# Optimization experiments

Hardware: AMD Instinct MI355X
Metric: run time of the kernel (lower is better)

Reference implementation:

```python
import jax, jax.numpy as jnp
import numpy as np

H = 64
VOCAB = 64
READ_FREQ = 16


def setup_inputs() -> dict:
    key = jax.random.key(0)
    ks = jax.random.split(key, 16)
    B, L, M = 512, 2048, 256
    seq = jax.random.randint(ks[0], (B, L), 0, VOCAB)
    memory = jax.random.normal(ks[1], (B, M, H), dtype=jnp.float32)
    s = 0.1
    return {
        "seq": seq,
        "memory": memory,
        "embed_w": jax.random.normal(ks[2], (VOCAB, H), jnp.float32) * s,
        "gru_w_ih": jax.random.normal(ks[3], (3 * H, 2 * H), jnp.float32) * s,
        "gru_w_hh": jax.random.normal(ks[4], (3 * H, H), jnp.float32) * s,
        "gru_b_ih": jax.random.normal(ks[5], (3 * H,), jnp.float32) * s,
        "gru_b_hh": jax.random.normal(ks[6], (3 * H,), jnp.float32) * s,
        "key_w": jax.random.normal(ks[7], (H, H), jnp.float32) * s,
        "key_b": jax.random.normal(ks[8], (H,), jnp.float32) * s,
        "val_w": jax.random.normal(ks[9], (H, H), jnp.float32) * s,
        "val_b": jax.random.normal(ks[10], (H,), jnp.float32) * s,
        "query_w": jax.random.normal(ks[11], (H, H), jnp.float32) * s,
        "query_b": jax.random.normal(ks[12], (H,), jnp.float32) * s,
        "head_w": jax.random.normal(ks[13], (VOCAB, H), jnp.float32) * s,
        "head_b": jax.random.normal(ks[14], (VOCAB,), jnp.float32) * s,
    }


def _forward(seq, memory, embed_w, gru_w_ih, gru_w_hh, gru_b_ih, gru_b_hh,
             key_w, key_b, val_w, val_b, query_w, query_b, head_w, head_b):
    B, L = seq.shape
    scale = 1.0 / (H ** 0.5)
    # memory is fixed: precompute keys/values once (B, M, H)
    k = jnp.einsum("bmh,kh->bmk", memory, key_w) + key_b
    v = jnp.einsum("bmh,kh->bmk", memory, val_w) + val_b
    # embed all tokens up front: (B, L, H) -> chunks (C, F, B, H)
    emb = embed_w[seq]
    C = L // READ_FREQ
    emb_chunks = emb.reshape(B, C, READ_FREQ, H).transpose(1, 2, 0, 3)

    def gru_step(carry, x_t):
        h, retrieved = carry
        inp = jnp.concatenate([x_t, retrieved], axis=-1)  # (B, 2H)
        gi = inp @ gru_w_ih.T + gru_b_ih                   # (B, 3H)
        gh = h @ gru_w_hh.T + gru_b_hh                     # (B, 3H)
        i_r, i_z, i_n = jnp.split(gi, 3, axis=-1)
        h_r, h_z, h_n = jnp.split(gh, 3, axis=-1)
        r = jax.nn.sigmoid(i_r + h_r)
        z = jax.nn.sigmoid(i_z + h_z)
        n = jnp.tanh(i_n + r * h_n)
        h_new = (1.0 - z) * n + z * h
        return (h_new, retrieved), None

    def chunk_step(h, chunk_emb):  # chunk_emb: (READ_FREQ, B, H)
        q = h @ query_w.T + query_b                        # (B, H)
        scores = jnp.einsum("bh,bmh->bm", q, k) * scale
        w = jax.nn.softmax(scores, axis=-1)
        retrieved = jnp.einsum("bm,bmh->bh", w, v)
        (h, _), _ = jax.lax.scan(gru_step, (h, retrieved), chunk_emb)
        return h, None

    h0 = jnp.zeros((B, H), dtype=memory.dtype)
    h, _ = jax.lax.scan(chunk_step, h0, emb_chunks)
    return h @ head_w.T + head_b                            # (B, VOCAB)


def reference(seq, memory, embed_w, gru_w_ih, gru_w_hh, gru_b_ih, gru_b_hh,
              key_w, key_b, val_w, val_b, query_w, query_b, head_w, head_b):
    return _forward(seq, memory, embed_w, gru_w_ih, gru_w_hh, gru_b_ih, gru_b_hh,
                    key_w, key_b, val_w, val_b, query_w, query_b, head_w, head_b)
```

## Files before the change

kernel.cpp:

```cpp
#include <hip/hip_runtime.h>
#include <hip/hip_fp16.h>


#define B_ 512
#define L_ 2048
#define M_ 256
#define H_ 64
#define C_ 128
#define F_ 16

typedef float v2f __attribute__((ext_vector_type(2)));
typedef _Float16 h2v __attribute__((ext_vector_type(2)));

#if __has_builtin(__builtin_amdgcn_fdot2)
__device__ __forceinline__ float FDOT2(h2v a, h2v b, float c) {
    return __builtin_amdgcn_fdot2(a, b, c, false);
}
#else
__device__ __forceinline__ float FDOT2(h2v a, h2v b, float c) {
    return c + (float)a[0]*(float)b[0] + (float)a[1]*(float)b[1];
}
#endif

__device__ __forceinline__ h2v bch(unsigned u) { return __builtin_bit_cast(h2v, u); }
__device__ __forceinline__ unsigned rl_u(unsigned v, int lane) {
    return (unsigned)__builtin_amdgcn_readlane((int)v, lane);
}
__device__ __forceinline__ float rl(float v, int lane) {
    return __int_as_float(__builtin_amdgcn_readlane(__float_as_int(v), lane));
}
__device__ __forceinline__ unsigned pkrtz(float a, float b) {
    auto r = __builtin_amdgcn_cvt_pkrtz(a, b);
    return __builtin_bit_cast(unsigned, r);
}
__device__ __forceinline__ float dot4(float4 a, float4 b) {
    return a.x*b.x + a.y*b.y + a.z*b.z + a.w*b.w;
}
__device__ __forceinline__ float fast_rcp(float x) { return __builtin_amdgcn_rcpf(x); }
__device__ __forceinline__ float sigm(float x) { return fast_rcp(1.f + __expf(-x)); }
__device__ __forceinline__ float tanh_f(float x) {
    float e2 = __expf(-2.f * fabsf(x));
    return copysignf((1.f - e2) * fast_rcp(1.f + e2), x);
}
__device__ __forceinline__ unsigned h2rn(float a, float b) {
    __half2 h = __floats2half2_rn(a, b);
    return __builtin_bit_cast(unsigned, h);
}

#define WS_KT    0u
#define WS_V     16777216u
#define WS_G     33554432u
#define WS_WPHH  33603584u
#define WS_WR    33628160u
#define WS_QP    33652736u
#define WS_KWP   33660928u
#define WS_VWP   33677312u
#define WS_KQF   33693696u
#define WS_BQ    33710080u
#define WS_KQV   33710336u
#define WS_C0    33710592u
#define WS_CB    33710848u

#define S_KT   0u
#define S_V    32768u
#define S_P    66560u
#define SMEM_BYTES 67072u

__global__ void pack_weights(const float* __restrict__ w_ih,
                             const float* __restrict__ w_hh,
                             const float* __restrict__ vw,
                             unsigned* __restrict__ WPhh2,
                             unsigned* __restrict__ WR2p,
                             float4* __restrict__ VWP)
{
    int idx = blockIdx.x * 256 + threadIdx.x;
    if (idx < 6144) {
        int j = idx & 63, t = idx >> 6, g = t % 3, k2 = t / 3;
        const float* s = w_hh + (g*64 + j)*64 + 2*k2;
        WPhh2[idx] = h2rn(s[0], s[1]);
    } else if (idx < 12288) {
        int i = idx - 6144;
        int j = i & 63, t = i >> 6, g = t % 3, k2 = t / 3;
        const float* s = w_ih + (g*64 + j)*128 + 64 + 2*k2;
        WR2p[i] = h2rn(s[0], s[1]);
    } else if (idx < 13312) {
        int i = idx - 12288;
        int j = i & 63, k4 = i >> 6;
        const float* s = vw + j*64 + 4*k4;
        VWP[i] = make_float4(s[0], s[1], s[2], s[3]);
    }
}

__global__ __launch_bounds__(64) void fold_kq(const float* __restrict__ kw,
                                              const float* __restrict__ qw,
                                              const float* __restrict__ kb,
                                              const float* __restrict__ qb,
                                              float* __restrict__ KQf,
                                              float* __restrict__ bqv,
                                              float* __restrict__ kqv,
                                              float* __restrict__ c0p)
{
    int d = blockIdx.x, j = threadIdx.x;
    __shared__ float kcol[64], kbs[64], qbs[64];
    kcol[j] = kw[j*64 + d];
    kbs[j]  = kb[j];
    qbs[j]  = qb[j];
    __syncthreads();
    float acc = 0.f, accq = 0.f;
    for (int t = 0; t < 64; ++t) {
        float kc = kcol[t];
        acc  += kc * qw[t*64 + j];
        accq += kc * qbs[t];
    }
    KQf[d*64 + j] = acc;
    if (j == 0) kqv[d] = accq;
    if (d == 0) {
        float vb = 0.f;
        for (int t = 0; t < 64; ++t) vb += kbs[t] * qw[t*64 + j];
        bqv[j] = vb;
        if (j == 0) {
            float c0 = 0.f;
            for (int t = 0; t < 64; ++t) c0 += kbs[t] * qbs[t];
            *c0p = c0;
        }
    }
}

__global__ __launch_bounds__(256) void pack_kq(const float* __restrict__ KQf,
                                               float4* __restrict__ KQP)
{
    int i = blockIdx.x * 256 + threadIdx.x;
    if (i < 1024) {
        int o = i & 63, k4 = i >> 6;
        KQP[i] = make_float4(KQf[(4*k4+0)*64 + o], KQf[(4*k4+1)*64 + o],
                             KQf[(4*k4+2)*64 + o], KQf[(4*k4+3)*64 + o]);
    }
}

__global__ __launch_bounds__(64) void build_G(const float* __restrict__ embed_w,
                                              const float* __restrict__ w_ih,
                                              const float* __restrict__ b_ih,
                                              float* __restrict__ G)
{
    int v = blockIdx.x, j = threadIdx.x;
    __shared__ float e_s[64];
    e_s[j] = embed_w[v*64 + j];
    __syncthreads();
    float a0 = b_ih[j], a1 = b_ih[64 + j], a2 = b_ih[128 + j];
    for (int k = 0; k < 64; ++k) {
        float e = e_s[k];
        a0 += e * w_ih[j*128 + k];
        a1 += e * w_ih[(64 + j)*128 + k];
        a2 += e * w_ih[(128 + j)*128 + k];
    }
    G[v*192 + j]       = a0;
    G[v*192 + 64 + j]  = a1;
    G[v*192 + 128 + j] = a2;
}

__global__ __launch_bounds__(256) void compute_kv(const float* __restrict__ memory,
                                                  const float* __restrict__ bqv,
                                                  const float* __restrict__ val_b,
                                                  const float4* __restrict__ KQP,
                                                  const float4* __restrict__ VWP,
                                                  const float* __restrict__ kqv,
                                                  const float* __restrict__ c0p,
                                                  unsigned* __restrict__ kT2,
                                                  unsigned* __restrict__ vT2,
                                                  float* __restrict__ cB)
{
    int wid = threadIdx.x >> 6;
    int o   = threadIdx.x & 63;
    int row = blockIdx.x * 4 + wid;
    int b = row >> 8, m = row & 255;
    __shared__ __align__(16) float mem_s[4][64];
    __shared__ float avs[4][64];
    mem_s[wid][o] = memory[(size_t)row * 64 + o];
    __syncthreads();
    float ak = bqv[o], av = val_b[o], ac = *c0p;
    const float4* m4  = (const float4*)mem_s[wid];
    const float4* kq4 = (const float4*)kqv;
#pragma unroll
    for (int k4 = 0; k4 < 16; ++k4) {
        float4 mm = m4[k4];
        ak += dot4(mm, KQP[k4*64 + o]);
        av += dot4(mm, VWP[k4*64 + o]);
        ac += dot4(mm, kq4[k4]);
    }
    float nb = __shfl_xor(ak, 1);
    if ((o & 1) == 0)
        kT2[((size_t)b*32 + (o >> 1))*256 + m] = h2rn(ak, nb);
    avs[wid][o] = av;
    if (o == 0) cB[row] = ac;
    __syncthreads();
    if ((wid & 1) == 0) {
        vT2[((size_t)b*64 + o)*128 + (m >> 1)] = h2rn(avs[wid][o], avs[wid+1][o]);
    }
}

#define GRU_STEP(cg0, cg1, cg2) do {                                        \
    float gr = RrB, gz = RzB, gn = bhn;                                     \
    _Pragma("unroll")                                                       \
    for (int kp = 0; kp < 32; ++kp) {                                       \
        h2v hhp = bch(rl_u(hpu, 2*kp));                                     \
        gr = FDOT2(hhp, wr2[kp], gr);                                       \
        gz = FDOT2(hhp, wz2[kp], gz);                                       \
        gn = FDOT2(hhp, wn2[kp], gn);                                       \
    }                                                                       \
    float r_ = sigm(gr + (cg0));                                            \
    float z_ = sigm(gz + (cg1));                                            \
    float n_ = tanh_f(((cg2) + Rn) + r_ * gn);                              \
    h = fmaf(z_, h - n_, n_);                                               \
    float hx_ = __shfl_xor(h, 1);                                           \
    hpu = pkrtz(h, hx_);                                                    \
} while (0)

__global__ __launch_bounds__(64, 1) void recurrent_main(
    const int*   __restrict__ seq,
    const float* __restrict__ b_hh,
    const float* __restrict__ head_w,
    const float* __restrict__ head_b,
    const unsigned* __restrict__ kT2g,
    const unsigned* __restrict__ vT2g,
    const float* __restrict__ G,
    const unsigned* __restrict__ WPhh2,
    const unsigned* __restrict__ WR2p,
    const float* __restrict__ cB,
    float* __restrict__ out)
{
    const int b = blockIdx.x;
    const int j = threadIdx.x;

    extern __shared__ __align__(16) char smem[];
    const uint4* kT2_lds = (const uint4*)(smem + S_KT);

    {
        const uint4* kTg = (const uint4*)(kT2g + (size_t)b * 8192);
        uint4* kTls = (uint4*)(smem + S_KT);
#pragma unroll
        for (int i = 0; i < 32; ++i) kTls[i*64 + j] = kTg[i*64 + j];
        const uint4* vg4 = (const uint4*)(vT2g + (size_t)b * 8192);
        uint4* vls4 = (uint4*)(smem + S_V);
#pragma unroll
        for (int i = 0; i < 32; ++i) {
            int t = i*64 + j;
            vls4[(t >> 5)*33 + (t & 31)] = vg4[t];
        }
    }

    h2v wr2[32], wz2[32], wn2[32];
#pragma unroll
    for (int k2 = 0; k2 < 32; ++k2) {
        wr2[k2] = bch(WPhh2[(k2*3 + 0)*64 + j]);
        wz2[k2] = bch(WPhh2[(k2*3 + 1)*64 + j]);
        wn2[k2] = bch(WPhh2[(k2*3 + 2)*64 + j]);
    }
    h2v rr2[32], rz2[32], rn2[32];
#pragma unroll
    for (int k2 = 0; k2 < 32; ++k2) {
        rr2[k2] = bch(WR2p[(k2*3 + 0)*64 + j]);
        rz2[k2] = bch(WR2p[(k2*3 + 1)*64 + j]);
        rn2[k2] = bch(WR2p[(k2*3 + 2)*64 + j]);
    }

    float h = 0.f;
    unsigned hpu = 0u;
    const float bhr = b_hh[j], bhz = b_hh[64 + j], bhn = b_hh[128 + j];
    const float4 cc = *(const float4*)(cB + (size_t)b*256 + 4*j);

    const int* seqb = seq + (size_t)b * L_;
    const uint4* vrow = (const uint4*)(smem + S_V) + j*33;
    const uint4* p4   = (const uint4*)(smem + S_P);
    __builtin_amdgcn_wave_barrier();

    for (int c = 0; c < C_; ++c) {
        const int c16 = c * F_;

        const int4 pA = *(const int4*)(seqb + c16);
        const int4 pB = *(const int4*)(seqb + c16 + 4);
        const int4 pC = *(const int4*)(seqb + c16 + 8);
        const int4 pD = *(const int4*)(seqb + c16 + 12);

        float s0 = cc.x, s1 = cc.y, s2 = cc.z, s3 = cc.w;
#pragma unroll 8
        for (int t = 0; t < 32; ++t) {
            h2v qq = bch(rl_u(hpu, 2*t));
            uint4 kk = kT2_lds[t*64 + j];
            s0 = FDOT2(bch(kk.x), qq, s0);
            s1 = FDOT2(bch(kk.y), qq, s1);
            s2 = FDOT2(bch(kk.z), qq, s2);
            s3 = FDOT2(bch(kk.w), qq, s3);
        }
        const float scale = 0.125f;
        float4 p;
        p.x = __expf(s0*scale); p.y = __expf(s1*scale);
        p.z = __expf(s2*scale); p.w = __expf(s3*scale);
        float sum = (p.x + p.y) + (p.z + p.w);
#pragma unroll
        for (int o = 32; o > 0; o >>= 1) sum += __shfl_xor(sum, o);
        float inv = fast_rcp(sum);
        *(uint2*)(smem + S_P + (size_t)j*8) =
            make_uint2(pkrtz(p.x, p.y), pkrtz(p.z, p.w));
        __builtin_amdgcn_wave_barrier();

        float r0 = 0.f, r1 = 0.f, r2 = 0.f, r3 = 0.f;
#pragma unroll 8
        for (int qd = 0; qd < 32; ++qd) {
            uint4 vv = vrow[qd];
            uint4 pp = p4[qd];
            r0 = FDOT2(bch(pp.x), bch(vv.x), r0);
            r1 = FDOT2(bch(pp.y), bch(vv.y), r1);
            r2 = FDOT2(bch(pp.z), bch(vv.z), r2);
            r3 = FDOT2(bch(pp.w), bch(vv.w), r3);
        }
        float ret = ((r0 + r1) + (r2 + r3)) * inv;

        float rx = __shfl_xor(ret, 1);
        unsigned rpu = pkrtz(ret, rx);
        float Rr = 0.f, Rz = 0.f, Rn = 0.f;
#pragma unroll
        for (int k2 = 0; k2 < 32; ++k2) {
            h2v rr = bch(rl_u(rpu, 2*k2));
            Rr = FDOT2(rr, rr2[k2], Rr);
            Rz = FDOT2(rr, rz2[k2], Rz);
            Rn = FDOT2(rr, rn2[k2], Rn);
        }
        const float RrB = Rr + bhr, RzB = Rz + bhz;

#pragma unroll 1
        for (int g = 0; g < 4; ++g) {
            const bool gb1 = (g & 1), gb2 = (g & 2);
            int4 tlo, thi, tg;
            tlo.x = gb1 ? pB.x : pA.x; tlo.y = gb1 ? pB.y : pA.y;
            tlo.z = gb1 ? pB.z : pA.z; tlo.w = gb1 ? pB.w : pA.w;
            thi.x = gb1 ? pD.x : pC.x; thi.y = gb1 ? pD.y : pC.y;
            thi.z = gb1 ? pD.z : pC.z; thi.w = gb1 ? pD.w : pC.w;
            tg.x = gb2 ? thi.x : tlo.x; tg.y = gb2 ? thi.y : tlo.y;
            tg.z = gb2 ? thi.z : tlo.z; tg.w = gb2 ? thi.w : tlo.w;
            const float* GA = G + tg.x*192;
            const float* GB = G + tg.y*192;
            const float* GC = G + tg.z*192;
            const float* GD = G + tg.w*192;
            float gA0 = GA[j], gA1 = GA[64+j], gA2 = GA[128+j];
            float gB0 = GB[j], gB1 = GB[64+j], gB2 = GB[128+j];
            float gC0 = GC[j], gC1 = GC[64+j], gC2 = GC[128+j];
            float gD0 = GD[j], gD1 = GD[64+j], gD2 = GD[128+j];

            GRU_STEP(gA0, gA1, gA2);
            GRU_STEP(gB0, gB1, gB2);
            GRU_STEP(gC0, gC1, gC2);
            GRU_STEP(gD0, gD1, gD2);
        }
    }

    float o = head_b[j];
#pragma unroll
    for (int k4 = 0; k4 < 16; ++k4) {
        float h0 = rl(h, 4*k4+0), h1 = rl(h, 4*k4+1);
        float h2 = rl(h, 4*k4+2), h3 = rl(h, 4*k4+3);
        const float* hw = head_w + j*64 + 4*k4;
        o += h0*hw[0] + h1*hw[1] + h2*hw[2] + h3*hw[3];
    }
    out[(size_t)b*64 + j] = o;
}

extern "C" void kernel_launch(void* const* d_in, const int* in_sizes, int n_in,
                              void* d_out, int out_size, void* d_ws, size_t ws_size,
                              hipStream_t stream) {
    const int*   seq      = (const int*)  d_in[0];
    const float* memory   = (const float*)d_in[1];
    const float* embed_w  = (const float*)d_in[2];
    const float* w_ih     = (const float*)d_in[3];
    const float* w_hh     = (const float*)d_in[4];
    const float* b_ih     = (const float*)d_in[5];
    const float* b_hh     = (const float*)d_in[6];
    const float* key_w    = (const float*)d_in[7];
    const float* key_b    = (const float*)d_in[8];
    const float* val_w    = (const float*)d_in[9];
    const float* val_b    = (const float*)d_in[10];
    const float* query_w  = (const float*)d_in[11];
    const float* query_b  = (const float*)d_in[12];
    const float* head_w   = (const float*)d_in[13];
    const float* head_b   = (const float*)d_in[14];

    char* ws = (char*)d_ws;
    unsigned* kT2  = (unsigned*)(ws + WS_KT);
    unsigned* vT2  = (unsigned*)(ws + WS_V);
    float*    G    = (float*)   (ws + WS_G);
    unsigned* WPhh2 = (unsigned*)(ws + WS_WPHH);
    unsigned* WR2p  = (unsigned*)(ws + WS_WR);
    float4*   KQP   = (float4*)  (ws + WS_KWP);
    float4*   VWP   = (float4*)  (ws + WS_VWP);
    float*    KQf   = (float*)   (ws + WS_KQF);
    float*    bqv   = (float*)   (ws + WS_BQ);
    float*    kqv   = (float*)   (ws + WS_KQV);
    float*    c0p   = (float*)   (ws + WS_C0);
    float*    cB    = (float*)   (ws + WS_CB);

    (void)hipFuncSetAttribute((const void*)recurrent_main,
                              hipFuncAttributeMaxDynamicSharedMemorySize,
                              (int)SMEM_BYTES);

    pack_weights<<<64, 256, 0, stream>>>(w_ih, w_hh, val_w, WPhh2, WR2p, VWP);
    fold_kq<<<64, 64, 0, stream>>>(key_w, query_w, key_b, query_b,
                                   KQf, bqv, kqv, c0p);
    pack_kq<<<4, 256, 0, stream>>>(KQf, KQP);
    build_G<<<64, 64, 0, stream>>>(embed_w, w_ih, b_ih, G);
    compute_kv<<<(B_*M_)/4, 256, 0, stream>>>(memory, bqv, val_b, KQP, VWP,
                                              kqv, c0p, kT2, vT2, cB);
    recurrent_main<<<B_, 64, SMEM_BYTES, stream>>>(seq, b_hh, head_w, head_b,
                                                   kT2, vT2, G, WPhh2, WR2p, cB,
                                                   (float*)d_out);
}
```

Measured before the change: 1.323 ms.

## Keep attention keys in registers and pack gate-input table as float4

Each thread now holds its 32 packed fp16 key vectors (128 VGPRs) in registers instead of reading them from LDS every chunk, which drops LDS use to only the value cache. Separately, the per-token gate-input table is repacked as one float4 per (token, unit) so each lookup is one 16-byte load instead of three scalar loads. The score loop is fully unrolled. This sharply raises register pressure in a kernel already holding 192 weight registers, risking spills, though occupancy is already one wave per block.

```diff
diff --git a/kernel.cpp b/kernel.cpp
--- a/kernel.cpp
+++ b/kernel.cpp
@@ -49,22 +49,20 @@
 
 #define WS_KT    0u
 #define WS_V     16777216u
-#define WS_G     33554432u
-#define WS_WPHH  33603584u
-#define WS_WR    33628160u
-#define WS_QP    33652736u
-#define WS_KWP   33660928u
-#define WS_VWP   33677312u
-#define WS_KQF   33693696u
-#define WS_BQ    33710080u
-#define WS_KQV   33710336u
-#define WS_C0    33710592u
-#define WS_CB    33710848u
-
-#define S_KT   0u
-#define S_V    32768u
-#define S_P    66560u
-#define SMEM_BYTES 67072u
+#define WS_G4    33554432u
+#define WS_WPHH  33619968u
+#define WS_WR    33644544u
+#define WS_KQP   33669120u
+#define WS_VWP   33685504u
+#define WS_KQF   33701888u
+#define WS_BQ    33718272u
+#define WS_KQV   33718528u
+#define WS_C0    33718784u
+#define WS_CB    33719040u
+
+#define S_V    0u
+#define S_P    33792u
+#define SMEM_BYTES 34304u
 
 __global__ void pack_weights(const float* __restrict__ w_ih,
                              const float* __restrict__ w_hh,
@@ -140,7 +138,7 @@
 __global__ __launch_bounds__(64) void build_G(const float* __restrict__ embed_w,
                                               const float* __restrict__ w_ih,
                                               const float* __restrict__ b_ih,
-                                              float* __restrict__ G)
+                                              float4* __restrict__ G4)
 {
     int v = blockIdx.x, j = threadIdx.x;
     __shared__ float e_s[64];
@@ -153,9 +151,7 @@
         a1 += e * w_ih[(64 + j)*128 + k];
         a2 += e * w_ih[(128 + j)*128 + k];
     }
-    G[v*192 + j]       = a0;
-    G[v*192 + 64 + j]  = a1;
-    G[v*192 + 128 + j] = a2;
+    G4[v*64 + j] = make_float4(a0, a1, a2, 0.f);
 }
 
 __global__ __launch_bounds__(256) void compute_kv(const float* __restrict__ memory,
@@ -222,7 +218,7 @@
     const float* __restrict__ head_b,
     const unsigned* __restrict__ kT2g,
     const unsigned* __restrict__ vT2g,
-    const float* __restrict__ G,
+    const float4* __restrict__ G4,
     const unsigned* __restrict__ WPhh2,
     const unsigned* __restrict__ WR2p,
     const float* __restrict__ cB,
@@ -232,13 +228,8 @@
     const int j = threadIdx.x;
 
     extern __shared__ __align__(16) char smem[];
-    const uint4* kT2_lds = (const uint4*)(smem + S_KT);
 
     {
-        const uint4* kTg = (const uint4*)(kT2g + (size_t)b * 8192);
-        uint4* kTls = (uint4*)(smem + S_KT);
-#pragma unroll
-        for (int i = 0; i < 32; ++i) kTls[i*64 + j] = kTg[i*64 + j];
         const uint4* vg4 = (const uint4*)(vT2g + (size_t)b * 8192);
         uint4* vls4 = (uint4*)(smem + S_V);
 #pragma unroll
@@ -246,6 +237,13 @@
             int t = i*64 + j;
             vls4[(t >> 5)*33 + (t & 31)] = vg4[t];
         }
+    }
+
+    uint4 kk[32];
+    {
+        const uint4* kTg = (const uint4*)(kT2g + (size_t)b * 8192);
+#pragma unroll
+        for (int t = 0; t < 32; ++t) kk[t] = kTg[t*64 + j];
     }
 
     h2v wr2[32], wz2[32], wn2[32];
@@ -282,14 +280,13 @@
         const int4 pD = *(const int4*)(seqb + c16 + 12);
 
         float s0 = cc.x, s1 = cc.y, s2 = cc.z, s3 = cc.w;
-#pragma unroll 8
+#pragma unroll
         for (int t = 0; t < 32; ++t) {
             h2v qq = bch(rl_u(hpu, 2*t));
-            uint4 kk = kT2_lds[t*64 + j];
-            s0 = FDOT2(bch(kk.x), qq, s0);
-            s1 = FDOT2(bch(kk.y), qq, s1);
-            s2 = FDOT2(bch(kk.z), qq, s2);
-            s3 = FDOT2(bch(kk.w), qq, s3);
+            s0 = FDOT2(bch(kk[t].x), qq, s0);
+            s1 = FDOT2(bch(kk[t].y), qq, s1);
+            s2 = FDOT2(bch(kk[t].z), qq, s2);
+            s3 = FDOT2(bch(kk[t].w), qq, s3);
         }
         const float scale = 0.125f;
         float4 p;
@@ -337,19 +334,15 @@
             thi.z = gb1 ? pD.z : pC.z; thi.w = gb1 ? pD.w : pC.w;
             tg.x = gb2 ? thi.x : tlo.x; tg.y = gb2 ? thi.y : tlo.y;
             tg.z = gb2 ? thi.z : tlo.z; tg.w = gb2 ? thi.w : tlo.w;
-            const float* GA = G + tg.x*192;
-            const float* GB = G + tg.y*192;
-            const float* GC = G + tg.z*192;
-            const float* GD = G + tg.w*192;
-            float gA0 = GA[j], gA1 = GA[64+j], gA2 = GA[128+j];
-            float gB0 = GB[j], gB1 = GB[64+j], gB2 = GB[128+j];
-            float gC0 = GC[j], gC1 = GC[64+j], gC2 = GC[128+j];
-            float gD0 = GD[j], gD1 = GD[64+j], gD2 = GD[128+j];
-
-            GRU_STEP(gA0, gA1, gA2);
-            GRU_STEP(gB0, gB1, gB2);
-            GRU_STEP(gC0, gC1, gC2);
-            GRU_STEP(gD0, gD1, gD2);
+            const float4 gA = G4[tg.x*64 + j];
+            const float4 gB = G4[tg.y*64 + j];
+            const float4 gC = G4[tg.z*64 + j];
+            const float4 gD = G4[tg.w*64 + j];
+
+            GRU_STEP(gA.x, gA.y, gA.z);
+            GRU_STEP(gB.x, gB.y, gB.z);
+            GRU_STEP(gC.x, gC.y, gC.z);
+            GRU_STEP(gD.x, gD.y, gD.z);
         }
     }
 
@@ -386,10 +379,10 @@
     char* ws = (char*)d_ws;
     unsigned* kT2  = (unsigned*)(ws + WS_KT);
     unsigned* vT2  = (unsigned*)(ws + WS_V);
-    float*    G    = (float*)   (ws + WS_G);
+    float4*   G4   = (float4*)  (ws + WS_G4);
     unsigned* WPhh2 = (unsigned*)(ws + WS_WPHH);
     unsigned* WR2p  = (unsigned*)(ws + WS_WR);
-    float4*   KQP   = (float4*)  (ws + WS_KWP);
+    float4*   KQP   = (float4*)  (ws + WS_KQP);
     float4*   VWP   = (float4*)  (ws + WS_VWP);
     float*    KQf   = (float*)   (ws + WS_KQF);
     float*    bqv   = (float*)   (ws + WS_BQ);
@@ -405,10 +398,10 @@
     fold_kq<<<64, 64, 0, stream>>>(key_w, query_w, key_b, query_b,
                                    KQf, bqv, kqv, c0p);
     pack_kq<<<4, 256, 0, stream>>>(KQf, KQP);
-    build_G<<<64, 64, 0, stream>>>(embed_w, w_ih, b_ih, G);
+    build_G<<<64, 64, 0, stream>>>(embed_w, w_ih, b_ih, G4);
     compute_kv<<<(B_*M_)/4, 256, 0, stream>>>(memory, bqv, val_b, KQP, VWP,
                                               kqv, c0p, kT2, vT2, cB);
     recurrent_main<<<B_, 64, SMEM_BYTES, stream>>>(seq, b_hh, head_w, head_b,
-                                                   kT2, vT2, G, WPhh2, WR2p, cB,
+                                                   kT2, vT2, G4, WPhh2, WR2p, cB,
                                                    (float*)d_out);
 }
```

New measurement: 1.446 ms. 9.3% more time.
